# Performance work log

Measured on AMD Instinct MI355X. Metric: run time of the kernel, lower is better.

The kernel has to match this reference:

```python
import jax, jax.numpy as jnp
import numpy as np

N_NODES = 50000
N_EDGES = 800000
F_IN = 128
HID = 256


def setup_inputs() -> dict:
    key = jax.random.key(0)
    ks = jax.random.split(key, 10)
    x = jax.random.normal(ks[0], (N_NODES, F_IN), jnp.float32)
    edge_index = jax.random.randint(ks[1], (2, N_EDGES), 0, N_NODES, jnp.int32)
    # Glorot-ish scaled weights (PyG Linear default init style)
    def w(k, o, i):
        return jax.random.normal(k, (o, i), jnp.float32) * (1.0 / np.sqrt(i))
    return {
        "x": x,
        "edge_index": edge_index,
        "W1l": w(ks[2], HID, F_IN), "b1l": jnp.zeros((HID,), jnp.float32),
        "W1r": w(ks[3], HID, F_IN),
        "W2l": w(ks[4], HID, HID), "b2l": jnp.zeros((HID,), jnp.float32),
        "W2r": w(ks[5], HID, HID),
        "Wh1": w(ks[6], 4, HID), "bh1": jnp.zeros((4,), jnp.float32),
        "Wh2": w(ks[7], 3, HID), "bh2": jnp.zeros((3,), jnp.float32),
    }


def sage_conv(x, edge_index, Wl, bl, Wr):
    # PyG SAGEConv (aggr='mean'): out_i = Wl @ mean_{j in N(i)} x_j + bl + Wr @ x_i
    src, dst = edge_index[0], edge_index[1]
    n = x.shape[0]
    summed = jax.ops.segment_sum(x[src], dst, num_segments=n)        # [N, F]
    cnt = jax.ops.segment_sum(jnp.ones((src.shape[0],), x.dtype), dst, num_segments=n)
    agg = summed / jnp.maximum(cnt, 1.0)[:, None]                    # isolated nodes -> 0
    return agg @ Wl.T + bl + x @ Wr.T


def reference(x, edge_index, W1l, b1l, W1r, W2l, b2l, W2r, Wh1, bh1, Wh2, bh2):
    h = jax.nn.relu(sage_conv(x, edge_index, W1l, b1l, W1r))
    # dropout(p=0.5) is identity in eval mode
    h = sage_conv(h, edge_index, W2l, b2l, W2r)
    out1 = h @ Wh1.T + bh1   # l2_classifier=False branch
    out2 = h @ Wh2.T + bh2
    return (out1, out2, h)
```

## Files before the change

### kernel.cpp

```cpp
#include <hip/hip_runtime.h>
#include <hip/hip_bf16.h>

typedef short bf16x8 __attribute__((ext_vector_type(8)));
typedef float f32x4 __attribute__((ext_vector_type(4)));

__device__ __forceinline__ float bf2f(__hip_bfloat16 v) { return __bfloat162float(v); }
__device__ __forceinline__ float sh2f(short s) {
    union { float f; unsigned u; } c; c.u = ((unsigned)(unsigned short)s) << 16; return c.f;
}
__device__ __forceinline__ short f2sh(float f) {
    __hip_bfloat16 b = __float2bfloat16(f); return *(short*)&b;
}

__global__ void detect_kernel(const unsigned short* __restrict__ xu, int* __restrict__ flag) {
    int lane = threadIdx.x;
    unsigned short u = xu[lane * 2];
    unsigned e = (u >> 7) & 0xFF;
    bool good = (u == 0) || (e >= 110 && e <= 137);
    unsigned long long m = __ballot(good);
    if (lane == 0) *flag = (__popcll(m) < 32) ? 1 : 0;
}

__device__ __forceinline__ float loadAny(const void* p, size_t i, int isf32) {
    return isf32 ? ((const float*)p)[i] : bf2f(((const __hip_bfloat16*)p)[i]);
}

__global__ void ingest_kernel(const void* __restrict__ src, __hip_bfloat16* __restrict__ dst,
                              int n4, const int* __restrict__ flag) {
    int isf32 = *flag;
    int t = blockIdx.x * blockDim.x + threadIdx.x;
    if (t >= n4) return;
    short4 o;
    if (isf32) {
        float4 v = ((const float4*)src)[t];
        o.x = f2sh(v.x); o.y = f2sh(v.y); o.z = f2sh(v.z); o.w = f2sh(v.w);
    } else {
        o = ((const short4*)src)[t];
    }
    ((short4*)dst)[t] = o;
}

__global__ void prep_kernel(const void* W1l, const void* W1r, const void* W2l, const void* W2r,
                            const void* b1l, const void* b2l, const void* Wh1, const void* Wh2,
                            const void* bh1, const void* bh2,
                            __hip_bfloat16* __restrict__ W1c, __hip_bfloat16* __restrict__ W2c,
                            __hip_bfloat16* __restrict__ sb, const int* __restrict__ flag) {
    int isf32 = *flag;
    int t = blockIdx.x * blockDim.x + threadIdx.x;
    if (t < 65536) {
        int n = t >> 8, k = t & 255;
        float v = (k < 128) ? loadAny(W1l, n * 128 + k, isf32)
                            : loadAny(W1r, n * 128 + (k - 128), isf32);
        W1c[t] = __float2bfloat16(v);
        return;
    }
    int u = t - 65536;
    if (u < 131072) {
        int n = u >> 9, k = u & 511;
        float v = (k < 256) ? loadAny(W2l, n * 256 + k, isf32)
                            : loadAny(W2r, n * 256 + (k - 256), isf32);
        W2c[u] = __float2bfloat16(v);
        return;
    }
    int s = u - 131072;
    float v;
    if      (s < 256)  v = loadAny(b1l, s, isf32);
    else if (s < 512)  v = loadAny(b2l, s - 256, isf32);
    else if (s < 1536) v = loadAny(Wh1, s - 512, isf32);
    else if (s < 2304) v = loadAny(Wh2, s - 1536, isf32);
    else if (s < 2308) v = loadAny(bh1, s - 2304, isf32);
    else if (s < 2311) v = loadAny(bh2, s - 2308, isf32);
    else return;
    sb[s] = __float2bfloat16(v);
}

__global__ void deg_kernel(const int* __restrict__ ei, int E, int* __restrict__ deg) {
    int t = blockIdx.x * blockDim.x + threadIdx.x;
    if (t >= E) return;
    atomicAdd(&deg[ei[E + t]], 1);
}

__global__ __launch_bounds__(256) void scanA_kernel(const int* __restrict__ deg,
                                                    int* __restrict__ off,
                                                    int* __restrict__ bsum, int N) {
    __shared__ int ts[256];
    int t = threadIdx.x;
    int base = blockIdx.x * 1024 + t * 4;
    int v0 = (base + 0 < N) ? deg[base + 0] : 0;
    int v1 = (base + 1 < N) ? deg[base + 1] : 0;
    int v2 = (base + 2 < N) ? deg[base + 2] : 0;
    int v3 = (base + 3 < N) ? deg[base + 3] : 0;
    int i0 = v0, i1 = i0 + v1, i2 = i1 + v2, i3 = i2 + v3;
    ts[t] = i3;
    __syncthreads();
    for (int d = 1; d < 256; d <<= 1) {
        int x = (t >= d) ? ts[t - d] : 0;
        __syncthreads();
        ts[t] += x;
        __syncthreads();
    }
    int excl = (t > 0) ? ts[t - 1] : 0;
    if (base + 0 < N) off[base + 1] = excl + i0;
    if (base + 1 < N) off[base + 2] = excl + i1;
    if (base + 2 < N) off[base + 3] = excl + i2;
    if (base + 3 < N) off[base + 4] = excl + i3;
    if (t == 255) bsum[blockIdx.x] = ts[255];
}

__global__ __launch_bounds__(1024) void scanB_kernel(int* __restrict__ bsum, int nb) {
    __shared__ int ts[1024];
    int t = threadIdx.x;
    ts[t] = (t < nb) ? bsum[t] : 0;
    __syncthreads();
    for (int d = 1; d < 1024; d <<= 1) {
        int x = (t >= d) ? ts[t - d] : 0;
        __syncthreads();
        ts[t] += x;
        __syncthreads();
    }
    if (t < nb) bsum[t] = (t > 0) ? ts[t - 1] : 0;
}

__global__ void addC_kernel(int* __restrict__ off, const int* __restrict__ bsum, int N) {
    int i = blockIdx.x * blockDim.x + threadIdx.x;
    if (i == 0) off[0] = 0;
    if (i < N) off[i + 1] += bsum[i >> 10];
}

__global__ void fill_kernel(const int* __restrict__ ei, int E,
                            const int* __restrict__ off, int* __restrict__ cursor,
                            int* __restrict__ srcs) {
    int t = blockIdx.x * blockDim.x + threadIdx.x;
    if (t >= E) return;
    int dst = ei[E + t];
    int pos = off[dst] + atomicAdd(&cursor[dst], 1);
    srcs[pos] = ei[t];
}

__global__ void gather1_kernel(const __hip_bfloat16* __restrict__ x,
                               const int* __restrict__ off, const int* __restrict__ srcs,
                               __hip_bfloat16* __restrict__ agg, int N) {
    int gid  = blockIdx.x * blockDim.x + threadIdx.x;
    int wid  = gid >> 6;
    int lane = threadIdx.x & 63;
    int node = wid * 2 + (lane >> 5);
    int t    = lane & 31;
    if (node >= N) return;
    int beg = off[node], end = off[node + 1];
    float a0 = 0.f, a1 = 0.f, a2 = 0.f, a3 = 0.f;
    const short4* xb = (const short4*)x;
    int e = beg;
    for (; e + 7 < end; e += 8) {
        short4 v[8];
#pragma unroll
        for (int j = 0; j < 8; j++) v[j] = xb[(size_t)srcs[e + j] * 32 + t];
#pragma unroll
        for (int j = 0; j < 8; j++) {
            a0 += sh2f(v[j].x); a1 += sh2f(v[j].y);
            a2 += sh2f(v[j].z); a3 += sh2f(v[j].w);
        }
    }
    for (; e < end; e++) {
        short4 v = xb[(size_t)srcs[e] * 32 + t];
        a0 += sh2f(v.x); a1 += sh2f(v.y); a2 += sh2f(v.z); a3 += sh2f(v.w);
    }
    float inv = 1.0f / fmaxf((float)(end - beg), 1.0f);
    short4 o;
    o.x = f2sh(a0 * inv); o.y = f2sh(a1 * inv);
    o.z = f2sh(a2 * inv); o.w = f2sh(a3 * inv);
    ((short4*)agg)[(size_t)node * 32 + t] = o;
}

__global__ void gather2_kernel(const __hip_bfloat16* __restrict__ h,
                               const int* __restrict__ off, const int* __restrict__ srcs,
                               __hip_bfloat16* __restrict__ agg, int N) {
    int node = (blockIdx.x * blockDim.x + threadIdx.x) >> 6;
    int lane = threadIdx.x & 63;
    if (node >= N) return;
    int beg = off[node], end = off[node + 1];
    float a0 = 0.f, a1 = 0.f, a2 = 0.f, a3 = 0.f;
    const short4* hb = (const short4*)h;
    int e = beg;
    for (; e + 7 < end; e += 8) {
        short4 v[8];
#pragma unroll
        for (int j = 0; j < 8; j++) v[j] = hb[(size_t)srcs[e + j] * 64 + lane];
#pragma unroll
        for (int j = 0; j < 8; j++) {
            a0 += sh2f(v[j].x); a1 += sh2f(v[j].y);
            a2 += sh2f(v[j].z); a3 += sh2f(v[j].w);
        }
    }
    for (; e < end; e++) {
        short4 v = hb[(size_t)srcs[e] * 64 + lane];
        a0 += sh2f(v.x); a1 += sh2f(v.y); a2 += sh2f(v.z); a3 += sh2f(v.w);
    }
    float inv = 1.0f / fmaxf((float)(end - beg), 1.0f);
    short4 o;
    o.x = f2sh(a0 * inv); o.y = f2sh(a1 * inv);
    o.z = f2sh(a2 * inv); o.w = f2sh(a3 * inv);
    ((short4*)agg)[(size_t)node * 64 + lane] = o;
}

struct AFrag { bf16x8 v[4]; };

template <int K, int KA, bool RELU, bool TOOUT>
__global__ __launch_bounds__(256) void gemm_lds(const __hip_bfloat16* __restrict__ A1,
                                                const __hip_bfloat16* __restrict__ A2, int M,
                                                const __hip_bfloat16* __restrict__ W,
                                                const __hip_bfloat16* __restrict__ bias,
                                                __hip_bfloat16* __restrict__ outb,
                                                void* __restrict__ dout,
                                                const int* __restrict__ flag) {
    __shared__ short wlds[32768];
    constexpr int KB = K - KA;
    constexpr int NCHUNK = K / 256;
    int tid  = threadIdx.x;
    int wave = tid >> 6, lane = tid & 63, quad = lane >> 4, l15 = lane & 15;
    int rowBlk = blockIdx.x >> 1, half = blockIdx.x & 1;
    int R0 = rowBlk * 256;
    int cbase = half * 128;

    int mrow[4];
#pragma unroll
    for (int rt = 0; rt < 4; rt++) mrow[rt] = min(R0 + wave * 64 + rt * 16 + l15, M - 1);

    const short* Ws = (const short*)W;

    auto loadW = [&](int p, bf16x8* wreg) {
#pragma unroll
        for (int i = 0; i < 16; i++) {
            int unit = tid + i * 256;
            int ln = unit & 63, nt = (unit >> 6) & 7, kt = unit >> 9;
            int row = cbase + nt * 16 + (ln & 15);
            int kk  = p * 256 + kt * 32 + (ln >> 4) * 8;
            wreg[i] = *(const bf16x8*)(Ws + (size_t)row * K + kk);
        }
    };
    auto storeW = [&](const bf16x8* wreg) {
#pragma unroll
        for (int i = 0; i < 16; i++) {
            int unit = tid + i * 256;
            *(bf16x8*)&wlds[unit * 8] = wreg[i];
        }
    };
    auto loadA = [&](int kglob) {
        AFrag f;
#pragma unroll
        for (int rt = 0; rt < 4; rt++) {
            const short* ap = (kglob < KA)
                ? (const short*)A1 + (size_t)mrow[rt] * KA + kglob + quad * 8
                : (const short*)A2 + (size_t)mrow[rt] * KB + (kglob - KA) + quad * 8;
            f.v[rt] = *(const bf16x8*)ap;
        }
        return f;
    };

    f32x4 acc[4][8];
#pragma unroll
    for (int rt = 0; rt < 4; rt++)
#pragma unroll
        for (int nt = 0; nt < 8; nt++) acc[rt][nt] = {0.f, 0.f, 0.f, 0.f};

    bf16x8 wreg[16];
    loadW(0, wreg);
    storeW(wreg);
    __syncthreads();
    AFrag a0f = loadA(0);
    AFrag a1f = loadA(32 < K ? 32 : 0);

    for (int p = 0; p < NCHUNK; p++) {
        if (p + 1 < NCHUNK) loadW(p + 1, wreg);
#pragma unroll
        for (int kt = 0; kt < 8; kt++) {
            int kg = p * 256 + kt * 32;
            int kg2 = kg + 64;
            if (kg2 > K - 32) kg2 = K - 32;
            AFrag a_next = loadA(kg2);
#pragma unroll
            for (int nt = 0; nt < 8; nt++) {
                bf16x8 b = *(const bf16x8*)&wlds[((kt * 8 + nt) * 64 + lane) * 8];
#pragma unroll
                for (int rt = 0; rt < 4; rt++)
                    acc[rt][nt] = __builtin_amdgcn_mfma_f32_16x16x32_bf16(a0f.v[rt], b, acc[rt][nt], 0, 0, 0);
            }
            a0f = a1f;
            a1f = a_next;
        }
        if (p + 1 < NCHUNK) {
            __syncthreads();
            storeW(wreg);
            __syncthreads();
        }
    }

    int isf32 = TOOUT ? *flag : 0;
    float* hf = TOOUT ? ((float*)dout + (size_t)M * 7) : nullptr;
    __hip_bfloat16* hb = TOOUT ? ((__hip_bfloat16*)dout + (size_t)M * 7) : outb;

#pragma unroll
    for (int rt = 0; rt < 4; rt++) {
#pragma unroll
        for (int nt = 0; nt < 8; nt++) {
            int col = cbase + nt * 16 + l15;
            float bv = bf2f(bias[col]);
#pragma unroll
            for (int r = 0; r < 4; r++) {
                int row = R0 + wave * 64 + rt * 16 + quad * 4 + r;
                if (row < M) {
                    float v = acc[rt][nt][r] + bv;
                    if (RELU) v = fmaxf(v, 0.f);
                    size_t idx = (size_t)row * 256 + col;
                    if (TOOUT && isf32) hf[idx] = v;
                    else                hb[idx] = __float2bfloat16(v);
                }
            }
        }
    }
}

__global__ void heads_kernel(const __hip_bfloat16* __restrict__ sb,
                             void* dout, int N, const int* __restrict__ flag) {
    int isf32 = *flag;
    int node = (blockIdx.x * blockDim.x + threadIdx.x) >> 6;
    int lane = threadIdx.x & 63;
    if (node >= N) return;
    float hv0, hv1, hv2, hv3;
    if (isf32) {
        const float4* hp = (const float4*)((const float*)dout + (size_t)N * 7);
        float4 v = hp[(size_t)node * 64 + lane];
        hv0 = v.x; hv1 = v.y; hv2 = v.z; hv3 = v.w;
    } else {
        const __hip_bfloat162* hp = (const __hip_bfloat162*)((const __hip_bfloat16*)dout + (size_t)N * 7);
        __hip_bfloat162 a = hp[(size_t)node * 128 + 2 * lane];
        __hip_bfloat162 b = hp[(size_t)node * 128 + 2 * lane + 1];
        hv0 = bf2f(a.x); hv1 = bf2f(a.y); hv2 = bf2f(b.x); hv3 = bf2f(b.y);
    }
#pragma unroll
    for (int r = 0; r < 7; r++) {
        const __hip_bfloat16* wrow = (r < 4) ? (sb + 512 + r * 256) : (sb + 1536 + (r - 4) * 256);
        const __hip_bfloat162* wr2 = (const __hip_bfloat162*)wrow;
        __hip_bfloat162 wa = wr2[2 * lane];
        __hip_bfloat162 wb = wr2[2 * lane + 1];
        float p = hv0 * bf2f(wa.x) + hv1 * bf2f(wa.y) + hv2 * bf2f(wb.x) + hv3 * bf2f(wb.y);
        for (int off = 32; off > 0; off >>= 1) p += __shfl_down(p, off, 64);
        if (lane == 0) {
            float bias = (r < 4) ? bf2f(sb[2304 + r]) : bf2f(sb[2308 + (r - 4)]);
            float v = p + bias;
            size_t idx = (r < 4) ? ((size_t)node * 4 + r)
                                 : ((size_t)N * 4 + (size_t)node * 3 + (r - 4));
            if (isf32) ((float*)dout)[idx] = v;
            else       ((__hip_bfloat16*)dout)[idx] = __float2bfloat16(v);
        }
    }
}

extern "C" void kernel_launch(void* const* d_in, const int* in_sizes, int n_in,
                              void* d_out, int out_size, void* d_ws, size_t ws_size,
                              hipStream_t stream) {
    const void* x   = d_in[0];
    const int*  ei  = (const int*)d_in[1];
    const void* W1l = d_in[2];
    const void* b1l = d_in[3];
    const void* W1r = d_in[4];
    const void* W2l = d_in[5];
    const void* b2l = d_in[6];
    const void* W2r = d_in[7];
    const void* Wh1 = d_in[8];
    const void* bh1 = d_in[9];
    const void* Wh2 = d_in[10];
    const void* bh2 = d_in[11];

    const int N = in_sizes[0] / 128;
    const int E = in_sizes[1] / 2;
    const int NB = (N + 1023) / 1024;

    char* ws = (char*)d_ws;
    int*            offp   = (int*)(ws + 0);
    int*            deg    = (int*)(ws + 262144);
    int*            cursor = (int*)(ws + 524288);
    int*            bsum   = (int*)(ws + 724992);
    int*            srcs   = (int*)(ws + 786432);
    __hip_bfloat16* W1c    = (__hip_bfloat16*)(ws + 3986432);
    __hip_bfloat16* W2c    = (__hip_bfloat16*)(ws + 4117504);
    __hip_bfloat16* sb     = (__hip_bfloat16*)(ws + 4379648);
    __hip_bfloat16* xn     = (__hip_bfloat16*)(ws + 4387840);
    __hip_bfloat16* h1     = (__hip_bfloat16*)(ws + 17187840);
    __hip_bfloat16* agg    = (__hip_bfloat16*)(ws + 42787840);
    int*            flag   = (int*)(ws + 68387840);

    hipMemsetAsync(ws + 262144, 0, 524288, stream);

    detect_kernel<<<1, 64, 0, stream>>>((const unsigned short*)x, flag);

    ingest_kernel<<<(N * 32 + 255) / 256, 256, 0, stream>>>(x, xn, N * 32, flag);
    prep_kernel<<<(65536 + 131072 + 2311 + 255) / 256, 256, 0, stream>>>(
        W1l, W1r, W2l, W2r, b1l, b2l, Wh1, Wh2, bh1, bh2, W1c, W2c, sb, flag);

    deg_kernel<<<(E + 255) / 256, 256, 0, stream>>>(ei, E, deg);
    scanA_kernel<<<NB, 256, 0, stream>>>(deg, offp, bsum, N);
    scanB_kernel<<<1, 1024, 0, stream>>>(bsum, NB);
    addC_kernel<<<(N + 255) / 256, 256, 0, stream>>>(offp, bsum, N);
    fill_kernel<<<(E + 255) / 256, 256, 0, stream>>>(ei, E, offp, cursor, srcs);

    const int rowBlks = (N + 255) / 256;

    {
        int waves = (N + 1) / 2;
        gather1_kernel<<<(waves * 64 + 255) / 256, 256, 0, stream>>>(xn, offp, srcs, agg, N);
    }
    gemm_lds<256, 128, true, false><<<rowBlks * 2, 256, 0, stream>>>(
        agg, xn, N, W1c, sb, h1, nullptr, flag);

    gather2_kernel<<<(N * 64 + 255) / 256, 256, 0, stream>>>(h1, offp, srcs, agg, N);
    gemm_lds<512, 256, false, true><<<rowBlks * 2, 256, 0, stream>>>(
        agg, h1, N, W2c, sb + 256, nullptr, d_out, flag);

    heads_kernel<<<(N + 3) / 4, 256, 0, stream>>>(sb, d_out, N, flag);
}
```

Measured before the change: 386.3 us.

## Fuse head projections into GEMM epilogue and drop fill-stage atomics

After: 360.6 us. -6.6%, faster.

```diff
diff --git a/kernel.cpp b/kernel.cpp
--- a/kernel.cpp
+++ b/kernel.cpp
@@ -74,10 +74,11 @@
     sb[s] = __float2bfloat16(v);
 }
 
-__global__ void deg_kernel(const int* __restrict__ ei, int E, int* __restrict__ deg) {
+__global__ void deg_kernel(const int* __restrict__ ei, int E, int* __restrict__ deg,
+                           int* __restrict__ rank) {
     int t = blockIdx.x * blockDim.x + threadIdx.x;
     if (t >= E) return;
-    atomicAdd(&deg[ei[E + t]], 1);
+    rank[t] = atomicAdd(&deg[ei[E + t]], 1);
 }
 
 __global__ __launch_bounds__(256) void scanA_kernel(const int* __restrict__ deg,
@@ -128,17 +129,18 @@
 }
 
 __global__ void fill_kernel(const int* __restrict__ ei, int E,
-                            const int* __restrict__ off, int* __restrict__ cursor,
-                            int* __restrict__ srcs) {
+                            const int* __restrict__ off, const int* __restrict__ rank,
+                            unsigned short* __restrict__ srcs) {
     int t = blockIdx.x * blockDim.x + threadIdx.x;
     if (t >= E) return;
     int dst = ei[E + t];
-    int pos = off[dst] + atomicAdd(&cursor[dst], 1);
-    srcs[pos] = ei[t];
+    int pos = off[dst] + rank[t];
+    srcs[pos] = (unsigned short)ei[t];
 }
 
 __global__ void gather1_kernel(const __hip_bfloat16* __restrict__ x,
-                               const int* __restrict__ off, const int* __restrict__ srcs,
+                               const int* __restrict__ off,
+                               const unsigned short* __restrict__ srcs,
                                __hip_bfloat16* __restrict__ agg, int N) {
     int gid  = blockIdx.x * blockDim.x + threadIdx.x;
     int wid  = gid >> 6;
@@ -172,7 +174,8 @@
 }
 
 __global__ void gather2_kernel(const __hip_bfloat16* __restrict__ h,
-                               const int* __restrict__ off, const int* __restrict__ srcs,
+                               const int* __restrict__ off,
+                               const unsigned short* __restrict__ srcs,
                                __hip_bfloat16* __restrict__ agg, int N) {
     int node = (blockIdx.x * blockDim.x + threadIdx.x) >> 6;
     int lane = threadIdx.x & 63;
@@ -211,7 +214,9 @@
                                                 const __hip_bfloat16* __restrict__ bias,
                                                 __hip_bfloat16* __restrict__ outb,
                                                 void* __restrict__ dout,
-                                                const int* __restrict__ flag) {
+                                                const int* __restrict__ flag,
+                                                const __hip_bfloat16* __restrict__ headW,
+                                                float* __restrict__ hpart) {
     __shared__ short wlds[32768];
     constexpr int KB = K - KA;
     constexpr int NCHUNK = K / 256;
@@ -300,59 +305,68 @@
 
 #pragma unroll
     for (int rt = 0; rt < 4; rt++) {
+        float hp[28];
+        if (TOOUT) {
+#pragma unroll
+            for (int i = 0; i < 28; i++) hp[i] = 0.f;
+        }
 #pragma unroll
         for (int nt = 0; nt < 8; nt++) {
             int col = cbase + nt * 16 + l15;
             float bv = bf2f(bias[col]);
+            float wv[7];
+            if (TOOUT) {
+#pragma unroll
+                for (int hh = 0; hh < 7; hh++) wv[hh] = bf2f(headW[hh * 256 + col]);
+            }
 #pragma unroll
             for (int r = 0; r < 4; r++) {
                 int row = R0 + wave * 64 + rt * 16 + quad * 4 + r;
+                float v = acc[rt][nt][r] + bv;
+                if (RELU) v = fmaxf(v, 0.f);
+                if (TOOUT) {
+#pragma unroll
+                    for (int hh = 0; hh < 7; hh++) hp[r * 7 + hh] += v * wv[hh];
+                }
                 if (row < M) {
-                    float v = acc[rt][nt][r] + bv;
-                    if (RELU) v = fmaxf(v, 0.f);
                     size_t idx = (size_t)row * 256 + col;
                     if (TOOUT && isf32) hf[idx] = v;
                     else                hb[idx] = __float2bfloat16(v);
                 }
             }
         }
-    }
-}
-
-__global__ void heads_kernel(const __hip_bfloat16* __restrict__ sb,
-                             void* dout, int N, const int* __restrict__ flag) {
+        if (TOOUT) {
+#pragma unroll
+            for (int r = 0; r < 4; r++) {
+                int row = R0 + wave * 64 + rt * 16 + quad * 4 + r;
+#pragma unroll
+                for (int hh = 0; hh < 7; hh++) {
+                    float s = hp[r * 7 + hh];
+                    s += __shfl_xor(s, 1, 64);
+                    s += __shfl_xor(s, 2, 64);
+                    s += __shfl_xor(s, 4, 64);
+                    s += __shfl_xor(s, 8, 64);
+                    if (l15 == 0 && row < M)
+                        hpart[((size_t)half * M + row) * 8 + hh] = s;
+                }
+            }
+        }
+    }
+}
+
+__global__ void head_final_kernel(const float* __restrict__ hpart,
+                                  const __hip_bfloat16* __restrict__ sb,
+                                  void* dout, int N, const int* __restrict__ flag) {
     int isf32 = *flag;
-    int node = (blockIdx.x * blockDim.x + threadIdx.x) >> 6;
-    int lane = threadIdx.x & 63;
-    if (node >= N) return;
-    float hv0, hv1, hv2, hv3;
-    if (isf32) {
-        const float4* hp = (const float4*)((const float*)dout + (size_t)N * 7);
-        float4 v = hp[(size_t)node * 64 + lane];
-        hv0 = v.x; hv1 = v.y; hv2 = v.z; hv3 = v.w;
-    } else {
-        const __hip_bfloat162* hp = (const __hip_bfloat162*)((const __hip_bfloat16*)dout + (size_t)N * 7);
-        __hip_bfloat162 a = hp[(size_t)node * 128 + 2 * lane];
-        __hip_bfloat162 b = hp[(size_t)node * 128 + 2 * lane + 1];
-        hv0 = bf2f(a.x); hv1 = bf2f(a.y); hv2 = bf2f(b.x); hv3 = bf2f(b.y);
-    }
-#pragma unroll
-    for (int r = 0; r < 7; r++) {
-        const __hip_bfloat16* wrow = (r < 4) ? (sb + 512 + r * 256) : (sb + 1536 + (r - 4) * 256);
-        const __hip_bfloat162* wr2 = (const __hip_bfloat162*)wrow;
-        __hip_bfloat162 wa = wr2[2 * lane];
-        __hip_bfloat162 wb = wr2[2 * lane + 1];
-        float p = hv0 * bf2f(wa.x) + hv1 * bf2f(wa.y) + hv2 * bf2f(wb.x) + hv3 * bf2f(wb.y);
-        for (int off = 32; off > 0; off >>= 1) p += __shfl_down(p, off, 64);
-        if (lane == 0) {
-            float bias = (r < 4) ? bf2f(sb[2304 + r]) : bf2f(sb[2308 + (r - 4)]);
-            float v = p + bias;
-            size_t idx = (r < 4) ? ((size_t)node * 4 + r)
-                                 : ((size_t)N * 4 + (size_t)node * 3 + (r - 4));
-            if (isf32) ((float*)dout)[idx] = v;
-            else       ((__hip_bfloat16*)dout)[idx] = __float2bfloat16(v);
-        }
-    }
+    int t = blockIdx.x * blockDim.x + threadIdx.x;
+    int node = t >> 3, hh = t & 7;
+    if (node >= N || hh >= 7) return;
+    float v = hpart[(size_t)node * 8 + hh] + hpart[((size_t)N + node) * 8 + hh]
+            + bf2f(sb[2304 + hh]);
+    size_t idx = (hh < 4) ? ((size_t)node * 4 + hh)
+                          : ((size_t)N * 4 + (size_t)node * 3 + (hh - 4));
+    if (isf32) ((float*)dout)[idx] = v;
+    else       ((__hip_bfloat16*)dout)[idx] = __float2bfloat16(v);
 }
 
 extern "C" void kernel_launch(void* const* d_in, const int* in_sizes, int n_in,
@@ -378,18 +392,19 @@
     char* ws = (char*)d_ws;
     int*            offp   = (int*)(ws + 0);
     int*            deg    = (int*)(ws + 262144);
-    int*            cursor = (int*)(ws + 524288);
-    int*            bsum   = (int*)(ws + 724992);
-    int*            srcs   = (int*)(ws + 786432);
+    int*            bsum   = (int*)(ws + 524288);
+    unsigned short* srcs   = (unsigned short*)(ws + 786432);
+    float*          hpart  = (float*)(ws + 786432);
     __hip_bfloat16* W1c    = (__hip_bfloat16*)(ws + 3986432);
     __hip_bfloat16* W2c    = (__hip_bfloat16*)(ws + 4117504);
     __hip_bfloat16* sb     = (__hip_bfloat16*)(ws + 4379648);
     __hip_bfloat16* xn     = (__hip_bfloat16*)(ws + 4387840);
     __hip_bfloat16* h1     = (__hip_bfloat16*)(ws + 17187840);
+    int*            rank   = (int*)(ws + 17187840);
     __hip_bfloat16* agg    = (__hip_bfloat16*)(ws + 42787840);
     int*            flag   = (int*)(ws + 68387840);
 
-    hipMemsetAsync(ws + 262144, 0, 524288, stream);
+    hipMemsetAsync(deg, 0, 204800, stream);
 
     detect_kernel<<<1, 64, 0, stream>>>((const unsigned short*)x, flag);
 
@@ -397,11 +412,11 @@
     prep_kernel<<<(65536 + 131072 + 2311 + 255) / 256, 256, 0, stream>>>(
         W1l, W1r, W2l, W2r, b1l, b2l, Wh1, Wh2, bh1, bh2, W1c, W2c, sb, flag);
 
-    deg_kernel<<<(E + 255) / 256, 256, 0, stream>>>(ei, E, deg);
+    deg_kernel<<<(E + 255) / 256, 256, 0, stream>>>(ei, E, deg, rank);
     scanA_kernel<<<NB, 256, 0, stream>>>(deg, offp, bsum, N);
     scanB_kernel<<<1, 1024, 0, stream>>>(bsum, NB);
     addC_kernel<<<(N + 255) / 256, 256, 0, stream>>>(offp, bsum, N);
-    fill_kernel<<<(E + 255) / 256, 256, 0, stream>>>(ei, E, offp, cursor, srcs);
+    fill_kernel<<<(E + 255) / 256, 256, 0, stream>>>(ei, E, offp, rank, srcs);
 
     const int rowBlks = (N + 255) / 256;
 
@@ -410,11 +425,11 @@
         gather1_kernel<<<(waves * 64 + 255) / 256, 256, 0, stream>>>(xn, offp, srcs, agg, N);
     }
     gemm_lds<256, 128, true, false><<<rowBlks * 2, 256, 0, stream>>>(
-        agg, xn, N, W1c, sb, h1, nullptr, flag);
+        agg, xn, N, W1c, sb, h1, nullptr, flag, nullptr, nullptr);
 
     gather2_kernel<<<(N * 64 + 255) / 256, 256, 0, stream>>>(h1, offp, srcs, agg, N);
     gemm_lds<512, 256, false, true><<<rowBlks * 2, 256, 0, stream>>>(
-        agg, h1, N, W2c, sb + 256, nullptr, d_out, flag);
-
-    heads_kernel<<<(N + 3) / 4, 256, 0, stream>>>(sb, d_out, N, flag);
-}
+        agg, h1, N, W2c, sb + 256, nullptr, d_out, flag, sb + 512, hpart);
+
+    head_final_kernel<<<(N * 8 + 255) / 256, 256, 0, stream>>>(hpart, sb, d_out, N, flag);
+}
```
